# Optimization experiments

Hardware: AMD Instinct MI355X
Metric: run time of the kernel (lower is better)

Reference implementation:

```python
import jax, jax.numpy as jnp
import numpy as np
from jax import lax

B, T, F, H, NC = 64, 256, 64, 128, 2


def setup_inputs() -> dict:
    key = jax.random.key(0)
    ks = jax.random.split(key, 10)
    # timestamps: sorted ints with duplicates -> exercises per-timestamp mean aggregation
    t = jnp.sort(jax.random.randint(ks[0], (B, T), 0, T // 2), axis=1).astype(jnp.float32)
    m = jax.random.randint(ks[1], (B, T), 0, F).astype(jnp.float32)
    x = jax.random.normal(ks[2], (B, T), dtype=jnp.float32)
    delt = jax.random.uniform(ks[3], (B, T), dtype=jnp.float32)
    X = jnp.stack([t, m, x, delt], axis=1)  # [B, 4, T]
    lengths = jax.random.randint(ks[4], (B,), T // 2, T + 1).astype(jnp.int32)
    s = 1.0 / np.sqrt(H + 1)
    W_lin = jax.random.uniform(ks[5], (F, H + 1, 4 * H), minval=-s, maxval=s, dtype=jnp.float32)
    b_lin = jax.random.uniform(ks[6], (F, 4 * H), minval=-s, maxval=s, dtype=jnp.float32)
    W_dec = jax.random.uniform(ks[7], (F,), minval=-1.0, maxval=1.0, dtype=jnp.float32)
    b_dec = jax.random.uniform(ks[8], (F,), minval=-1.0, maxval=1.0, dtype=jnp.float32)
    so = 1.0 / np.sqrt(F * H + H)
    k9, k10 = jax.random.split(ks[9])
    W_out = jax.random.uniform(k9, (F * H + H, NC), minval=-so, maxval=so, dtype=jnp.float32)
    b_out = jax.random.uniform(k10, (NC,), minval=-so, maxval=so, dtype=jnp.float32)
    return {"X": X, "lengths": lengths, "W_lin": W_lin, "b_lin": b_lin,
            "W_dec": W_dec, "b_dec": b_dec, "W_out": W_out, "b_out": b_out}


def _forward(X, lengths, W_lin, b_lin, W_dec, b_dec, W_out, b_out):
    nF, Hp1, H4 = W_lin.shape
    hs = Hp1 - 1
    t = X[:, 0]
    m = X[:, 1].astype(jnp.int32)
    x = X[:, 2]
    delt = X[:, 3]
    idx = jnp.arange(t.shape[1])
    valid = idx[None, :] < lengths[:, None]                       # event is real
    t_next = jnp.concatenate([t[:, 1:], t[:, -1:] + 1.0], axis=1)
    # last event of a consecutive-equal-timestamp group (within valid length)
    boundary = (idx[None, :] == (lengths[:, None] - 1)) | (t_next != t)

    def per_sample(m_s, x_s, d_s, v_s, b_s):
        def step(carry, inp):
            h_t, c_t, acc, cnt = carry
            mj, xj, dj, vj, bj = inp
            # feature-specific decay of that feature's hidden row
            dm = W_dec[mj] * dj + b_dec[mj]
            decay = jnp.exp(-jnp.maximum(0.0, dm))
            h_dec = decay * h_t[mj]
            inp_vec = jnp.concatenate([xj[None], h_dec])          # [H+1]
            gates = inp_vec @ W_lin[mj] + b_lin[mj]               # [4H]
            gi, gf, go, gc = jnp.split(gates, 4)
            c_cand = jax.nn.sigmoid(gf) * c_t + jax.nn.sigmoid(gi) * jnp.tanh(gc)
            h_row = jax.nn.sigmoid(go) * jnp.tanh(c_cand)
            h_t = jnp.where(vj, h_t.at[mj].set(h_row), h_t)
            acc = acc + jnp.where(vj, c_cand, 0.0)
            cnt = cnt + jnp.where(vj, 1.0, 0.0)
            close = vj & bj                                       # end of timestamp group
            c_t = jnp.where(close, acc / jnp.maximum(cnt, 1.0), c_t)
            acc = jnp.where(close, jnp.zeros_like(acc), acc)
            cnt = jnp.where(close, 0.0, cnt)
            return (h_t, c_t, acc, cnt), None

        init = (jnp.zeros((nF, hs), jnp.float32), jnp.zeros((hs,), jnp.float32),
                jnp.zeros((hs,), jnp.float32), jnp.float32(0.0))
        (h_t, c_t, _, _), _ = lax.scan(step, init, (m_s, x_s, d_s, v_s, b_s))
        feats = jnp.concatenate([c_t, h_t.reshape(-1)])           # [H + F*H]
        return jax.nn.softmax(feats @ W_out + b_out)

    return jax.vmap(per_sample)(m, x, delt, valid, boundary)      # [B, n_class]


def reference(X, lengths, W_lin, b_lin, W_dec, b_dec, W_out, b_out):
    return _forward(X, lengths, W_lin, b_lin, W_dec, b_dec, W_out, b_out)
```

## Files before the change

### kernel.cpp

```cpp
#include <hip/hip_runtime.h>
#include <math.h>
#include <stdint.h>

#define BATCH 64
#define T 256
#define NF 64
#define H 128
#define H4 512
#define HP1 129
#define WF_STRIDE (HP1 * H4)
#define FEATS (NF * H + H)
#define NTH2 512

#define RING_SLOT 32768
#define PACK2_U4 (64 * 8 * 2 * 4 * 64)
#define PACK2_BYTES ((size_t)PACK2_U4 * 16u)
#define HDR2_BYTES  (64u * 512u * 16u)
#define WS_NEED ((size_t)HDR2_BYTES + PACK2_BYTES)

typedef float vf2 __attribute__((ext_vector_type(2)));

__device__ __forceinline__ float sigmoidf_(float x) {
    return 1.0f / (1.0f + __expf(-x));
}

__device__ __forceinline__ float tanhf_(float x) {
    float ax = fabsf(x);
    float e = __expf(2.0f * ax);
    float r = 1.0f - 2.0f / (e + 1.0f);
    return copysignf(r, x);
}

template<bool HI>
__device__ __forceinline__ vf2 dec2f(unsigned u) {
    return __builtin_amdgcn_cvt_pk_f32_fp8(u, HI);
}

__device__ __forceinline__ void dma16(const void* g, uint32_t lds_byte) {
    __builtin_amdgcn_global_load_lds(
        (const __attribute__((address_space(1))) void*)g,
        (__attribute__((address_space(3))) void*)(uintptr_t)lds_byte,
        16, 0, 0);
}

#define WAITV(N) do { asm volatile("s_waitcnt vmcnt(" #N ")" ::: "memory"); \
                      __builtin_amdgcn_sched_barrier(0); } while (0)
#define LGKM0()  do { asm volatile("s_waitcnt lgkmcnt(0)" ::: "memory"); \
                      __builtin_amdgcn_sched_barrier(0); } while (0)
#define BARRIER() do { asm volatile("s_waitcnt lgkmcnt(0)" ::: "memory"); \
                       __builtin_amdgcn_s_barrier(); \
                       asm volatile("" ::: "memory"); } while (0)

__global__ __launch_bounds__(256)
void repack2_kernel(const float* __restrict__ W_lin, uint4* __restrict__ pack2) {
    const int lin = blockIdx.x * 256 + threadIdx.x;
    const int l   = lin & 63;
    const int i   = (lin >> 6) & 3;
    const int Xv  = (lin >> 8) & 1;
    const int wv  = (lin >> 9) & 7;
    const int f   = lin >> 12;
    const int h   = wv * 16 + (l & 15);
    const int ks  = l >> 4;
    const int g   = Xv * 2 + (i >> 1);
    const int ksub = i & 1;
    const int col = g * 128 + h;
    const int k0  = ks * 32 + ksub * 16;
    const float* src = W_lin + (size_t)f * WF_STRIDE + (size_t)(1 + k0) * H4 + col;
    unsigned u[4];
    #pragma unroll
    for (int dw = 0; dw < 4; ++dw) {
        const float v0 = src[(4 * dw + 0) * H4] * 4096.0f;
        const float v1 = src[(4 * dw + 1) * H4] * 4096.0f;
        const float v2 = src[(4 * dw + 2) * H4] * 4096.0f;
        const float v3 = src[(4 * dw + 3) * H4] * 4096.0f;
        unsigned r = 0;
        r = __builtin_amdgcn_cvt_pk_fp8_f32(v0, v1, r, false);
        r = __builtin_amdgcn_cvt_pk_fp8_f32(v2, v3, r, true);
        u[dw] = r;
    }
    uint4 o; o.x = u[0]; o.y = u[1]; o.z = u[2]; o.w = u[3];
    pack2[lin] = o;
}

__global__ __launch_bounds__(256)
void hdr2_kernel(const float* __restrict__ W_lin, const float* __restrict__ b_lin,
                 uint4* __restrict__ hdr2) {
    const int lin = blockIdx.x * 256 + threadIdx.x;
    const int t2 = lin & 511, f = lin >> 9;
    const int wv = t2 >> 6, l = t2 & 63;
    const int h  = wv * 16 + (l & 15);
    union { uint4 u; _Float16 hf[8]; } o;
    #pragma unroll
    for (int g = 0; g < 4; ++g) {
        o.hf[g]     = (_Float16)W_lin[(size_t)f * WF_STRIDE + g * 128 + h];
        o.hf[4 + g] = (_Float16)b_lin[f * H4 + g * 128 + h];
    }
    hdr2[lin] = o.u;
}

__global__ __launch_bounds__(NTH2)
void lstm_scan_fp8_w1(const float* __restrict__ X,
                      const int* __restrict__ lengths,
                      const float* __restrict__ W_dec,
                      const float* __restrict__ b_dec,
                      const float* __restrict__ W_out,
                      const float* __restrict__ b_out,
                      const uint4* __restrict__ pack2,
                      const uint4* __restrict__ hdr2,
                      float* __restrict__ out)
{
    __shared__ __align__(16) char s_wb[3 * RING_SLOT];
    __shared__ __align__(16) char s_hd[2 * 8192];
    __shared__ float s_ht[NF * H];
    __shared__ float s_inp[H];
    __shared__ float s_X[4 * T];
    __shared__ float s_wdec[NF];
    __shared__ float s_bdec[NF];
    __shared__ float s_cfin[H];
    __shared__ float s_red[16];

    const int tid = threadIdx.x;
    const int b   = blockIdx.x;
    const int w   = tid >> 6;
    const int l   = tid & 63;
    const int h   = w * 16 + (l & 15);
    const int ks  = l >> 4;

    const float* Xb = X + b * 4 * T;
    const int len = lengths[b];

    for (int i = tid; i < NF * H; i += NTH2) s_ht[i] = 0.0f;
    for (int i = tid; i < 4 * T; i += NTH2) s_X[i] = Xb[i];
    if (tid < NF) { s_wdec[tid] = W_dec[tid]; s_bdec[tid] = b_dec[tid]; }
    if (tid < H) s_inp[tid] = 0.0f;
    __syncthreads();

    const uint32_t wb0 = (uint32_t)(uintptr_t)s_wb;
    const uint32_t hd0 = (uint32_t)(uintptr_t)s_hd;
    const uint32_t wbase  = __builtin_amdgcn_readfirstlane(wb0 + (uint32_t)w * 4096u);
    const uint32_t hdbase = __builtin_amdgcn_readfirstlane(hd0 + (uint32_t)w * 1024u);

    float c_t = 0.0f, accv = 0.0f, cntv = 0.0f;

    #define ISSUE_W4(mf, Xv, slot) do {                                          \
        const uint4* gp = pack2 + ((((size_t)(mf) * 8 + w) * 2 + (Xv)) * 4) * 64 + l; \
        const uint32_t dst = wbase + (uint32_t)(slot) * RING_SLOT;               \
        dma16(gp,       dst);                                                    \
        dma16(gp + 64,  dst + 1024u);                                            \
        dma16(gp + 128, dst + 2048u);                                            \
        dma16(gp + 192, dst + 3072u);                                            \
    } while (0)

    #define ISSUE_HDR(jj) do {                                                   \
        const int ss = ((jj) < T) ? (jj) : (T - 1);                              \
        const int mf = (int)s_X[T + ss];                                         \
        const uint4* gh = hdr2 + (size_t)mf * 512 + (w * 64 + l);                \
        dma16(gh, hdbase + (((jj) & 1) ? 8192u : 0u));                           \
    } while (0)

    #define DOTQ(Wq, G, KS) do {                                                 \
        const int pb = (KS) * 8;                                                 \
        vf2 d;                                                                   \
        d = dec2f<false>((Wq).x); acc[G] += d * iv[pb + 0];                      \
        d = dec2f<true >((Wq).x); acc[G] += d * iv[pb + 1];                      \
        d = dec2f<false>((Wq).y); acc[G] += d * iv[pb + 2];                      \
        d = dec2f<true >((Wq).y); acc[G] += d * iv[pb + 3];                      \
        d = dec2f<false>((Wq).z); acc[G] += d * iv[pb + 4];                      \
        d = dec2f<true >((Wq).z); acc[G] += d * iv[pb + 5];                      \
        d = dec2f<false>((Wq).w); acc[G] += d * iv[pb + 6];                      \
        d = dec2f<true >((Wq).w); acc[G] += d * iv[pb + 7];                      \
    } while (0)

    #define HALFX(Xv, slot) do {                                                 \
        uint4 q0, q1, q2, q3;                                                    \
        const uint32_t ra = wb0 + (uint32_t)(slot) * RING_SLOT                   \
                          + (uint32_t)w * 4096u + (uint32_t)l * 16u;             \
        asm volatile("ds_read_b128 %0, %4 offset:0\n\t"                          \
                     "ds_read_b128 %1, %4 offset:1024\n\t"                       \
                     "ds_read_b128 %2, %4 offset:2048\n\t"                       \
                     "ds_read_b128 %3, %4 offset:3072"                           \
                     : "=&v"(q0), "=&v"(q1), "=&v"(q2), "=&v"(q3)                \
                     : "v"(ra) : "memory");                                      \
        asm volatile("s_waitcnt lgkmcnt(0)" ::: "memory");                       \
        __builtin_amdgcn_sched_barrier(0);                                       \
        DOTQ(q0, (Xv) * 2 + 0, 0);                                               \
        DOTQ(q1, (Xv) * 2 + 0, 1);                                               \
        DOTQ(q2, (Xv) * 2 + 1, 0);                                               \
        DOTQ(q3, (Xv) * 2 + 1, 1);                                               \
    } while (0)

    {
        const int m0 = (int)s_X[T];
        ISSUE_W4(m0, 0, 0);
        ISSUE_HDR(0);
        ISSUE_W4(m0, 1, 1);
    }

    int r0 = 0;
    for (int j = 0; j < len; ++j) {
        const int   mj  = (int)s_X[T + j];
        const float xj  = s_X[2 * T + j];
        const int   jn  = (j + 1 < T) ? (j + 1) : (T - 1);
        const int   mjn = (int)s_X[T + jn];
        int r1 = r0 + 1; if (r1 >= 3) r1 -= 3;
        int r2 = r0 + 2; if (r2 >= 3) r2 -= 3;

        ISSUE_W4(mjn, 0, r2);
        ISSUE_HDR(j + 1);

        vf2 iv[16];
        {
            const float4* ip = (const float4*)(s_inp + ks * 32);
            #pragma unroll
            for (int q = 0; q < 8; ++q) {
                const float4 t = ip[q];
                iv[2 * q][0] = t.x;  iv[2 * q][1] = t.y;
                iv[2 * q + 1][0] = t.z; iv[2 * q + 1][1] = t.w;
            }
        }
        vf2 acc[4];
        #pragma unroll
        for (int g = 0; g < 4; ++g) { acc[g][0] = 0.0f; acc[g][1] = 0.0f; }

        WAITV(9);
        HALFX(0, r0);

        uint4 hb;
        {
            const uint32_t ha = hd0 + ((j & 1) ? 8192u : 0u)
                              + (uint32_t)w * 1024u + (uint32_t)l * 16u;
            asm volatile("ds_read_b128 %0, %1" : "=&v"(hb) : "v"(ha) : "memory");
        }
        LGKM0();
        ISSUE_W4(mjn, 1, r0);
        WAITV(9);
        HALFX(1, r1);

        union { uint4 u; _Float16 hf[8]; } hu; hu.u = hb;
        float gate[4];
        #pragma unroll
        for (int g = 0; g < 4; ++g) {
            float s = acc[g][0] + acc[g][1];
            s += __shfl_xor(s, 16, 64);
            s += __shfl_xor(s, 32, 64);
            gate[g] = fmaf(s, 1.0f / 4096.0f,
                           fmaf(xj, (float)hu.hf[g], (float)hu.hf[4 + g]));
        }
        const float c_cand = sigmoidf_(gate[1]) * c_t + sigmoidf_(gate[0]) * tanhf_(gate[3]);
        const float h_row  = sigmoidf_(gate[2]) * tanhf_(c_cand);
        accv += c_cand;
        cntv += 1.0f;
        const float tj = s_X[j];
        const float tn = (j < T - 1) ? s_X[j + 1] : (tj + 1.0f);
        const bool boundary = (j == len - 1) || (tn != tj);
        if (boundary) { c_t = accv / fmaxf(cntv, 1.0f); accv = 0.0f; cntv = 0.0f; }
        if ((l & 48) == 0) {
            s_ht[mj * H + h] = h_row;
            const float dn  = s_X[3 * T + jn];
            const float dmn = fmaf(s_wdec[mjn], dn, s_bdec[mjn]);
            const float den = __expf(-fmaxf(0.0f, dmn));
            const float hv  = (mjn == mj) ? h_row : s_ht[mjn * H + h];
            s_inp[h] = den * hv;
        }
        BARRIER();
        r0 = r2;
    }
    #undef HALFX
    #undef DOTQ
    #undef ISSUE_HDR
    #undef ISSUE_W4

    asm volatile("s_waitcnt vmcnt(0) lgkmcnt(0)" ::: "memory");
    __syncthreads();

    if ((l & 48) == 0) s_cfin[h] = c_t;
    __syncthreads();

    float z0 = 0.0f, z1 = 0.0f;
    for (int i = tid; i < FEATS; i += NTH2) {
        const float f = (i < H) ? s_cfin[i] : s_ht[i - H];
        const float2 wo = *(const float2*)(W_out + 2 * i);
        z0 = fmaf(f, wo.x, z0);
        z1 = fmaf(f, wo.y, z1);
    }
    #pragma unroll
    for (int off = 32; off > 0; off >>= 1) {
        z0 += __shfl_down(z0, off, 64);
        z1 += __shfl_down(z1, off, 64);
    }
    if (l == 0) { s_red[2 * w] = z0; s_red[2 * w + 1] = z1; }
    __syncthreads();
    if (tid == 0) {
        float a0 = b_out[0], a1 = b_out[1];
        #pragma unroll
        for (int q = 0; q < 8; ++q) { a0 += s_red[2 * q]; a1 += s_red[2 * q + 1]; }
        const float mx = fmaxf(a0, a1);
        const float e0 = __expf(a0 - mx), e1 = __expf(a1 - mx);
        const float inv = 1.0f / (e0 + e1);
        out[2 * b]     = e0 * inv;
        out[2 * b + 1] = e1 * inv;
    }
}

#define NTHREADS 512
__global__ __launch_bounds__(NTHREADS)
void lstm_scan_kernel(const float* __restrict__ X,
                      const int* __restrict__ lengths,
                      const float* __restrict__ W_lin,
                      const float* __restrict__ b_lin,
                      const float* __restrict__ W_dec,
                      const float* __restrict__ b_dec,
                      const float* __restrict__ W_out,
                      const float* __restrict__ b_out,
                      float* __restrict__ out)
{
    __shared__ float s_feats[FEATS];
    __shared__ float s_inp[H];
    __shared__ float s_part[4][H4];
    __shared__ float s_X[4 * T];
    __shared__ float s_wdec[NF];
    __shared__ float s_bdec[NF];
    __shared__ float s_red[16];

    float* s_ct = s_feats;
    float* s_ht = s_feats + H;

    const int tid = threadIdx.x;
    const int b   = blockIdx.x;
    const int g4  = tid & 127;
    const int kq  = tid >> 7;

    const float* Xb = X + b * 4 * T;
    const int len = lengths[b];

    for (int i = tid; i < NF * H; i += NTHREADS) s_ht[i] = 0.0f;
    for (int i = tid; i < 4 * T; i += NTHREADS) s_X[i] = Xb[i];
    if (tid < NF) { s_wdec[tid] = W_dec[tid]; s_bdec[tid] = b_dec[tid]; }
    __syncthreads();

    float c_t = 0.0f, acc = 0.0f, cnt = 0.0f;

    for (int j = 0; j < len; ++j) {
        const int   mj = (int)s_X[T + j];
        const float xj = s_X[2 * T + j];
        const float* Wf = W_lin + mj * WF_STRIDE;

        float bl0, bl1, bl2, bl3;
        if (tid < H) {
            const float dj    = s_X[3 * T + j];
            const float dm    = fmaf(s_wdec[mj], dj, s_bdec[mj]);
            const float decay = __expf(-fmaxf(0.0f, dm));
            s_inp[tid] = decay * s_ht[mj * H + tid];
            const int m4 = mj * H4;
            bl0 = b_lin[m4 + tid];
            bl1 = b_lin[m4 + H + tid];
            bl2 = b_lin[m4 + 2 * H + tid];
            bl3 = b_lin[m4 + 3 * H + tid];
        }
        __syncthreads();

        float4 a4 = make_float4(0.0f, 0.0f, 0.0f, 0.0f);
        {
            const float*  wr  = Wf + (1 + kq * 32) * H4 + 4 * g4;
            const float4* ivp = (const float4*)(s_inp + kq * 32);
            #pragma unroll
            for (int cc = 0; cc < 8; ++cc) {
                const float4 v = ivp[cc];
                const float* wrc = wr + (4 * cc) * H4;
                const float4 w0 = *(const float4*)(wrc);
                const float4 w1 = *(const float4*)(wrc + H4);
                const float4 w2 = *(const float4*)(wrc + 2 * H4);
                const float4 w3 = *(const float4*)(wrc + 3 * H4);
                a4.x = fmaf(v.x, w0.x, a4.x); a4.y = fmaf(v.x, w0.y, a4.y);
                a4.z = fmaf(v.x, w0.z, a4.z); a4.w = fmaf(v.x, w0.w, a4.w);
                a4.x = fmaf(v.y, w1.x, a4.x); a4.y = fmaf(v.y, w1.y, a4.y);
                a4.z = fmaf(v.y, w1.z, a4.z); a4.w = fmaf(v.y, w1.w, a4.w);
                a4.x = fmaf(v.z, w2.x, a4.x); a4.y = fmaf(v.z, w2.y, a4.y);
                a4.z = fmaf(v.z, w2.z, a4.z); a4.w = fmaf(v.z, w2.w, a4.w);
                a4.x = fmaf(v.w, w3.x, a4.x); a4.y = fmaf(v.w, w3.y, a4.y);
                a4.z = fmaf(v.w, w3.z, a4.z); a4.w = fmaf(v.w, w3.w, a4.w);
            }
        }
        if (kq == 0) {
            const float4 wv = *(const float4*)(Wf + 4 * g4);
            a4.x = fmaf(xj, wv.x, a4.x); a4.y = fmaf(xj, wv.y, a4.y);
            a4.z = fmaf(xj, wv.z, a4.z); a4.w = fmaf(xj, wv.w, a4.w);
        }
        *(float4*)(&s_part[kq][4 * g4]) = a4;
        __syncthreads();

        if (tid < H) {
            const int h = tid;
            const float gi = s_part[0][h]         + s_part[1][h]         + s_part[2][h]         + s_part[3][h]         + bl0;
            const float gf = s_part[0][H + h]     + s_part[1][H + h]     + s_part[2][H + h]     + s_part[3][H + h]     + bl1;
            const float go = s_part[0][2*H + h]   + s_part[1][2*H + h]   + s_part[2][2*H + h]   + s_part[3][2*H + h]   + bl2;
            const float gc = s_part[0][3*H + h]   + s_part[1][3*H + h]   + s_part[2][3*H + h]   + s_part[3][3*H + h]   + bl3;

            const float c_cand = sigmoidf_(gf) * c_t + sigmoidf_(gi) * tanhf_(gc);
            const float h_row  = sigmoidf_(go) * tanhf_(c_cand);
            s_ht[mj * H + h] = h_row;
            acc += c_cand;
            cnt += 1.0f;

            const float tj = s_X[j];
            const float tn = (j < T - 1) ? s_X[j + 1] : (tj + 1.0f);
            const bool boundary = (j == len - 1) || (tn != tj);
            if (boundary) { c_t = acc / fmaxf(cnt, 1.0f); acc = 0.0f; cnt = 0.0f; }
        }
        __syncthreads();
    }

    if (tid < H) s_ct[tid] = c_t;
    __syncthreads();

    float z0 = 0.0f, z1 = 0.0f;
    for (int i = tid; i < FEATS; i += NTHREADS) {
        const float f = s_feats[i];
        const float2 wv = *(const float2*)(W_out + 2 * i);
        z0 = fmaf(f, wv.x, z0);
        z1 = fmaf(f, wv.y, z1);
    }
    #pragma unroll
    for (int off = 32; off > 0; off >>= 1) {
        z0 += __shfl_down(z0, off, 64);
        z1 += __shfl_down(z1, off, 64);
    }
    const int wave = tid >> 6, lane = tid & 63;
    if (lane == 0) { s_red[2 * wave] = z0; s_red[2 * wave + 1] = z1; }
    __syncthreads();
    if (tid == 0) {
        float a0 = b_out[0], a1 = b_out[1];
        #pragma unroll
        for (int q = 0; q < 8; ++q) { a0 += s_red[2 * q]; a1 += s_red[2 * q + 1]; }
        const float mx = fmaxf(a0, a1);
        const float e0 = __expf(a0 - mx), e1 = __expf(a1 - mx);
        const float inv = 1.0f / (e0 + e1);
        out[2 * b]     = e0 * inv;
        out[2 * b + 1] = e1 * inv;
    }
}

extern "C" void kernel_launch(void* const* d_in, const int* in_sizes, int n_in,
                              void* d_out, int out_size, void* d_ws, size_t ws_size,
                              hipStream_t stream) {
    const float* X      = (const float*)d_in[0];
    const int*   lens   = (const int*)d_in[1];
    const float* W_lin  = (const float*)d_in[2];
    const float* b_lin  = (const float*)d_in[3];
    const float* W_dec  = (const float*)d_in[4];
    const float* b_dec  = (const float*)d_in[5];
    const float* W_out  = (const float*)d_in[6];
    const float* b_out  = (const float*)d_in[7];
    float* out = (float*)d_out;

    if (ws_size >= WS_NEED) {
        uint4* hdr2 = (uint4*)d_ws;
        uint4* pack2 = (uint4*)((char*)d_ws + HDR2_BYTES);
        hipLaunchKernelGGL(hdr2_kernel, dim3(128), dim3(256), 0, stream,
                           W_lin, b_lin, hdr2);
        hipLaunchKernelGGL(repack2_kernel, dim3(PACK2_U4 / 256), dim3(256), 0, stream,
                           W_lin, pack2);
        hipLaunchKernelGGL(lstm_scan_fp8_w1, dim3(BATCH), dim3(NTH2), 0, stream,
                           X, lens, W_dec, b_dec, W_out, b_out, pack2, hdr2, out);
    } else {
        hipLaunchKernelGGL(lstm_scan_kernel, dim3(BATCH), dim3(NTHREADS), 0, stream,
                           X, lens, W_lin, b_lin, W_dec, b_dec, W_out, b_out, out);
    }
}
```

Baseline: 507.6 us.

## Process two timesteps per iteration speculatively with two 512-thread groups

Replaces the single-step LSTM scan, which used an async LDS ring buffer for the weights, with a 1024-thread kernel. Two thread groups compute the matvecs for steps j and j+1 in parallel, and the second step is recomputed only when both steps hit the same feature row. Weights now load straight from global memory into registers instead of through the DMA prefetch ring. This halves the serial step count when features differ, at the cost of losing the prefetch overlap, adding extra barriers on collisions, and using larger blocks.

```diff
diff --git a/kernel.cpp b/kernel.cpp
--- a/kernel.cpp
+++ b/kernel.cpp
@@ -10,9 +10,8 @@
 #define HP1 129
 #define WF_STRIDE (HP1 * H4)
 #define FEATS (NF * H + H)
-#define NTH2 512
-
-#define RING_SLOT 32768
+#define NTH3 1024
+
 #define PACK2_U4 (64 * 8 * 2 * 4 * 64)
 #define PACK2_BYTES ((size_t)PACK2_U4 * 16u)
 #define HDR2_BYTES  (64u * 512u * 16u)
@@ -35,21 +34,6 @@
 __device__ __forceinline__ vf2 dec2f(unsigned u) {
     return __builtin_amdgcn_cvt_pk_f32_fp8(u, HI);
 }
-
-__device__ __forceinline__ void dma16(const void* g, uint32_t lds_byte) {
-    __builtin_amdgcn_global_load_lds(
-        (const __attribute__((address_space(1))) void*)g,
-        (__attribute__((address_space(3))) void*)(uintptr_t)lds_byte,
-        16, 0, 0);
-}
-
-#define WAITV(N) do { asm volatile("s_waitcnt vmcnt(" #N ")" ::: "memory"); \
-                      __builtin_amdgcn_sched_barrier(0); } while (0)
-#define LGKM0()  do { asm volatile("s_waitcnt lgkmcnt(0)" ::: "memory"); \
-                      __builtin_amdgcn_sched_barrier(0); } while (0)
-#define BARRIER() do { asm volatile("s_waitcnt lgkmcnt(0)" ::: "memory"); \
-                       __builtin_amdgcn_s_barrier(); \
-                       asm volatile("" ::: "memory"); } while (0)
 
 __global__ __launch_bounds__(256)
 void repack2_kernel(const float* __restrict__ W_lin, uint4* __restrict__ pack2) {
@@ -98,186 +82,197 @@
     hdr2[lin] = o.u;
 }
 
-__global__ __launch_bounds__(NTH2)
-void lstm_scan_fp8_w1(const float* __restrict__ X,
-                      const int* __restrict__ lengths,
-                      const float* __restrict__ W_dec,
-                      const float* __restrict__ b_dec,
-                      const float* __restrict__ W_out,
-                      const float* __restrict__ b_out,
-                      const uint4* __restrict__ pack2,
-                      const uint4* __restrict__ hdr2,
-                      float* __restrict__ out)
+__global__ __launch_bounds__(NTH3, 4)
+void lstm_scan_fp8_pair(const float* __restrict__ X,
+                        const int* __restrict__ lengths,
+                        const float* __restrict__ W_dec,
+                        const float* __restrict__ b_dec,
+                        const float* __restrict__ W_out,
+                        const float* __restrict__ b_out,
+                        const uint4* __restrict__ pack2,
+                        const uint4* __restrict__ hdr2,
+                        float* __restrict__ out)
 {
-    __shared__ __align__(16) char s_wb[3 * RING_SLOT];
-    __shared__ __align__(16) char s_hd[2 * 8192];
     __shared__ float s_ht[NF * H];
-    __shared__ float s_inp[H];
+    __shared__ float s_inpA[H];
+    __shared__ float s_inpB[H];
+    __shared__ float s_gates[2][H][4];
     __shared__ float s_X[4 * T];
     __shared__ float s_wdec[NF];
     __shared__ float s_bdec[NF];
     __shared__ float s_cfin[H];
-    __shared__ float s_red[16];
+    __shared__ float s_red[32];
 
     const int tid = threadIdx.x;
     const int b   = blockIdx.x;
-    const int w   = tid >> 6;
+    const int grp = tid >> 9;
+    const int w8  = (tid >> 6) & 7;
     const int l   = tid & 63;
-    const int h   = w * 16 + (l & 15);
+    const int h   = w8 * 16 + (l & 15);
     const int ks  = l >> 4;
 
     const float* Xb = X + b * 4 * T;
     const int len = lengths[b];
 
-    for (int i = tid; i < NF * H; i += NTH2) s_ht[i] = 0.0f;
-    for (int i = tid; i < 4 * T; i += NTH2) s_X[i] = Xb[i];
+    for (int i = tid; i < NF * H; i += NTH3) s_ht[i] = 0.0f;
+    for (int i = tid; i < 4 * T; i += NTH3) s_X[i] = Xb[i];
     if (tid < NF) { s_wdec[tid] = W_dec[tid]; s_bdec[tid] = b_dec[tid]; }
-    if (tid < H) s_inp[tid] = 0.0f;
-    __syncthreads();
-
-    const uint32_t wb0 = (uint32_t)(uintptr_t)s_wb;
-    const uint32_t hd0 = (uint32_t)(uintptr_t)s_hd;
-    const uint32_t wbase  = __builtin_amdgcn_readfirstlane(wb0 + (uint32_t)w * 4096u);
-    const uint32_t hdbase = __builtin_amdgcn_readfirstlane(hd0 + (uint32_t)w * 1024u);
+    if (tid < H) { s_inpA[tid] = 0.0f; s_inpB[tid] = 0.0f; }
+    __syncthreads();
 
     float c_t = 0.0f, accv = 0.0f, cntv = 0.0f;
 
-    #define ISSUE_W4(mf, Xv, slot) do {                                          \
-        const uint4* gp = pack2 + ((((size_t)(mf) * 8 + w) * 2 + (Xv)) * 4) * 64 + l; \
-        const uint32_t dst = wbase + (uint32_t)(slot) * RING_SLOT;               \
-        dma16(gp,       dst);                                                    \
-        dma16(gp + 64,  dst + 1024u);                                            \
-        dma16(gp + 128, dst + 2048u);                                            \
-        dma16(gp + 192, dst + 3072u);                                            \
+    #define DOTQ(Wq, G, KS) do {                                                \
+        const int pb = (KS) * 8;                                                \
+        vf2 d;                                                                  \
+        d = dec2f<false>((Wq).x); acc[G] += d * iv[pb + 0];                     \
+        d = dec2f<true >((Wq).x); acc[G] += d * iv[pb + 1];                     \
+        d = dec2f<false>((Wq).y); acc[G] += d * iv[pb + 2];                     \
+        d = dec2f<true >((Wq).y); acc[G] += d * iv[pb + 3];                     \
+        d = dec2f<false>((Wq).z); acc[G] += d * iv[pb + 4];                     \
+        d = dec2f<true >((Wq).z); acc[G] += d * iv[pb + 5];                     \
+        d = dec2f<false>((Wq).w); acc[G] += d * iv[pb + 6];                     \
+        d = dec2f<true >((Wq).w); acc[G] += d * iv[pb + 7];                     \
     } while (0)
 
-    #define ISSUE_HDR(jj) do {                                                   \
-        const int ss = ((jj) < T) ? (jj) : (T - 1);                              \
-        const int mf = (int)s_X[T + ss];                                         \
-        const uint4* gh = hdr2 + (size_t)mf * 512 + (w * 64 + l);                \
-        dma16(gh, hdbase + (((jj) & 1) ? 8192u : 0u));                           \
+    #define MATVEC(MF, INP, XV, GATE) do {                                      \
+        uint4 q[8];                                                             \
+        const uint4* wp_ = pack2 + (((size_t)(MF) * 8 + w8) * 2 * 4) * 64 + l;  \
+        _Pragma("unroll")                                                       \
+        for (int ii = 0; ii < 8; ++ii) q[ii] = wp_[ii * 64];                    \
+        union { uint4 u; _Float16 hf[8]; } hu_;                                 \
+        hu_.u = hdr2[(size_t)(MF) * 512 + (w8 * 64 + l)];                       \
+        vf2 iv[16];                                                             \
+        {                                                                       \
+            const float4* ip_ = (const float4*)((INP) + ks * 32);               \
+            _Pragma("unroll")                                                   \
+            for (int qd = 0; qd < 8; ++qd) {                                    \
+                const float4 t_ = ip_[qd];                                      \
+                iv[2 * qd][0] = t_.x;     iv[2 * qd][1] = t_.y;                 \
+                iv[2 * qd + 1][0] = t_.z; iv[2 * qd + 1][1] = t_.w;             \
+            }                                                                   \
+        }                                                                       \
+        vf2 acc[4];                                                             \
+        _Pragma("unroll")                                                       \
+        for (int g = 0; g < 4; ++g) { acc[g][0] = 0.0f; acc[g][1] = 0.0f; }     \
+        _Pragma("unroll")                                                       \
+        for (int Xi = 0; Xi < 2; ++Xi) {                                        \
+            DOTQ(q[Xi * 4 + 0], Xi * 2 + 0, 0);                                 \
+            DOTQ(q[Xi * 4 + 1], Xi * 2 + 0, 1);                                 \
+            DOTQ(q[Xi * 4 + 2], Xi * 2 + 1, 0);                                 \
+            DOTQ(q[Xi * 4 + 3], Xi * 2 + 1, 1);                                 \
+        }                                                                       \
+        _Pragma("unroll")                                                       \
+        for (int g = 0; g < 4; ++g) {                                           \
+            float s_ = acc[g][0] + acc[g][1];                                   \
+            s_ += __shfl_xor(s_, 16, 64);                                       \
+            s_ += __shfl_xor(s_, 32, 64);                                       \
+            GATE[g] = fmaf(s_, 1.0f / 4096.0f,                                  \
+                           fmaf((XV), (float)hu_.hf[g], (float)hu_.hf[4 + g])); \
+        }                                                                       \
     } while (0)
 
-    #define DOTQ(Wq, G, KS) do {                                                 \
-        const int pb = (KS) * 8;                                                 \
-        vf2 d;                                                                   \
-        d = dec2f<false>((Wq).x); acc[G] += d * iv[pb + 0];                      \
-        d = dec2f<true >((Wq).x); acc[G] += d * iv[pb + 1];                      \
-        d = dec2f<false>((Wq).y); acc[G] += d * iv[pb + 2];                      \
-        d = dec2f<true >((Wq).y); acc[G] += d * iv[pb + 3];                      \
-        d = dec2f<false>((Wq).z); acc[G] += d * iv[pb + 4];                      \
-        d = dec2f<true >((Wq).z); acc[G] += d * iv[pb + 5];                      \
-        d = dec2f<false>((Wq).w); acc[G] += d * iv[pb + 6];                      \
-        d = dec2f<true >((Wq).w); acc[G] += d * iv[pb + 7];                      \
-    } while (0)
-
-    #define HALFX(Xv, slot) do {                                                 \
-        uint4 q0, q1, q2, q3;                                                    \
-        const uint32_t ra = wb0 + (uint32_t)(slot) * RING_SLOT                   \
-                          + (uint32_t)w * 4096u + (uint32_t)l * 16u;             \
-        asm volatile("ds_read_b128 %0, %4 offset:0\n\t"                          \
-                     "ds_read_b128 %1, %4 offset:1024\n\t"                       \
-                     "ds_read_b128 %2, %4 offset:2048\n\t"                       \
-                     "ds_read_b128 %3, %4 offset:3072"                           \
-                     : "=&v"(q0), "=&v"(q1), "=&v"(q2), "=&v"(q3)                \
-                     : "v"(ra) : "memory");                                      \
-        asm volatile("s_waitcnt lgkmcnt(0)" ::: "memory");                       \
-        __builtin_amdgcn_sched_barrier(0);                                       \
-        DOTQ(q0, (Xv) * 2 + 0, 0);                                               \
-        DOTQ(q1, (Xv) * 2 + 0, 1);                                               \
-        DOTQ(q2, (Xv) * 2 + 1, 0);                                               \
-        DOTQ(q3, (Xv) * 2 + 1, 1);                                               \
-    } while (0)
-
-    {
-        const int m0 = (int)s_X[T];
-        ISSUE_W4(m0, 0, 0);
-        ISSUE_HDR(0);
-        ISSUE_W4(m0, 1, 1);
-    }
-
-    int r0 = 0;
-    for (int j = 0; j < len; ++j) {
-        const int   mj  = (int)s_X[T + j];
+    for (int j = 0; j < len; j += 2) {
+        const int  vj1 = (j + 1 < len);
+        const int  mj  = (int)s_X[T + j];
+        const int  j1c = (j + 1 < T) ? (j + 1) : (T - 1);
+        const int  mj1 = (int)s_X[T + j1c];
         const float xj  = s_X[2 * T + j];
-        const int   jn  = (j + 1 < T) ? (j + 1) : (T - 1);
-        const int   mjn = (int)s_X[T + jn];
-        int r1 = r0 + 1; if (r1 >= 3) r1 -= 3;
-        int r2 = r0 + 2; if (r2 >= 3) r2 -= 3;
-
-        ISSUE_W4(mjn, 0, r2);
-        ISSUE_HDR(j + 1);
-
-        vf2 iv[16];
+        const float xj1 = s_X[2 * T + j1c];
+
         {
-            const float4* ip = (const float4*)(s_inp + ks * 32);
-            #pragma unroll
-            for (int q = 0; q < 8; ++q) {
-                const float4 t = ip[q];
-                iv[2 * q][0] = t.x;  iv[2 * q][1] = t.y;
-                iv[2 * q + 1][0] = t.z; iv[2 * q + 1][1] = t.w;
+            const int   myM   = grp ? mj1 : mj;
+            const float myx   = grp ? xj1 : xj;
+            const float* myin = grp ? s_inpB : s_inpA;
+            float gate[4];
+            MATVEC(myM, myin, myx, gate);
+            if (ks == 0) {
+                float4 g4; g4.x = gate[0]; g4.y = gate[1]; g4.z = gate[2]; g4.w = gate[3];
+                *(float4*)&s_gates[grp][h][0] = g4;
             }
         }
-        vf2 acc[4];
-        #pragma unroll
-        for (int g = 0; g < 4; ++g) { acc[g][0] = 0.0f; acc[g][1] = 0.0f; }
-
-        WAITV(9);
-        HALFX(0, r0);
-
-        uint4 hb;
+        __syncthreads();
+
+        const float4 gA = *(const float4*)&s_gates[0][h][0];
+        float4 gB = *(const float4*)&s_gates[1][h][0];
+
+        const float c_candA = sigmoidf_(gA.y) * c_t + sigmoidf_(gA.x) * tanhf_(gA.w);
+        const float h_rowA  = sigmoidf_(gA.z) * tanhf_(c_candA);
+        accv += c_candA;
+        cntv += 1.0f;
         {
-            const uint32_t ha = hd0 + ((j & 1) ? 8192u : 0u)
-                              + (uint32_t)w * 1024u + (uint32_t)l * 16u;
-            asm volatile("ds_read_b128 %0, %1" : "=&v"(hb) : "v"(ha) : "memory");
-        }
-        LGKM0();
-        ISSUE_W4(mjn, 1, r0);
-        WAITV(9);
-        HALFX(1, r1);
-
-        union { uint4 u; _Float16 hf[8]; } hu; hu.u = hb;
-        float gate[4];
-        #pragma unroll
-        for (int g = 0; g < 4; ++g) {
-            float s = acc[g][0] + acc[g][1];
-            s += __shfl_xor(s, 16, 64);
-            s += __shfl_xor(s, 32, 64);
-            gate[g] = fmaf(s, 1.0f / 4096.0f,
-                           fmaf(xj, (float)hu.hf[g], (float)hu.hf[4 + g]));
-        }
-        const float c_cand = sigmoidf_(gate[1]) * c_t + sigmoidf_(gate[0]) * tanhf_(gate[3]);
-        const float h_row  = sigmoidf_(gate[2]) * tanhf_(c_cand);
-        accv += c_cand;
-        cntv += 1.0f;
-        const float tj = s_X[j];
-        const float tn = (j < T - 1) ? s_X[j + 1] : (tj + 1.0f);
-        const bool boundary = (j == len - 1) || (tn != tj);
-        if (boundary) { c_t = accv / fmaxf(cntv, 1.0f); accv = 0.0f; cntv = 0.0f; }
-        if ((l & 48) == 0) {
-            s_ht[mj * H + h] = h_row;
-            const float dn  = s_X[3 * T + jn];
-            const float dmn = fmaf(s_wdec[mjn], dn, s_bdec[mjn]);
-            const float den = __expf(-fmaxf(0.0f, dmn));
-            const float hv  = (mjn == mj) ? h_row : s_ht[mjn * H + h];
-            s_inp[h] = den * hv;
-        }
-        BARRIER();
-        r0 = r2;
-    }
-    #undef HALFX
+            const float tj  = s_X[j];
+            const float tn1 = (j < T - 1) ? s_X[j + 1] : (tj + 1.0f);
+            const bool bdry = (j == len - 1) || (tn1 != tj);
+            if (bdry) { c_t = accv / fmaxf(cntv, 1.0f); accv = 0.0f; cntv = 0.0f; }
+        }
+
+        const bool coll = vj1 && (mj1 == mj);
+        if (coll) {
+            const float d1  = s_X[3 * T + j1c];
+            const float dm1 = fmaf(s_wdec[mj1], d1, s_bdec[mj1]);
+            const float de1 = __expf(-fmaxf(0.0f, dm1));
+            if (grp == 1 && ks == 0) s_inpB[h] = de1 * h_rowA;
+            __syncthreads();
+            if (grp == 1) {
+                float gr[4];
+                MATVEC(mj1, s_inpB, xj1, gr);
+                if (ks == 0) {
+                    float4 g4; g4.x = gr[0]; g4.y = gr[1]; g4.z = gr[2]; g4.w = gr[3];
+                    *(float4*)&s_gates[1][h][0] = g4;
+                }
+            }
+            __syncthreads();
+            gB = *(const float4*)&s_gates[1][h][0];
+        }
+
+        float h_rowB = 0.0f;
+        if (vj1) {
+            const float c_candB = sigmoidf_(gB.y) * c_t + sigmoidf_(gB.x) * tanhf_(gB.w);
+            h_rowB = sigmoidf_(gB.z) * tanhf_(c_candB);
+            accv += c_candB;
+            cntv += 1.0f;
+            const float tj1 = s_X[j1c];
+            const float tn2 = (j + 1 < T - 1) ? s_X[j + 2] : (tj1 + 1.0f);
+            const bool bdry = (j + 1 == len - 1) || (tn2 != tj1);
+            if (bdry) { c_t = accv / fmaxf(cntv, 1.0f); accv = 0.0f; cntv = 0.0f; }
+        }
+
+        if (ks == 0) {
+            if (grp == 0 && !coll) s_ht[mj * H + h] = h_rowA;
+            if (grp == 1 && vj1)   s_ht[mj1 * H + h] = h_rowB;
+        }
+
+        const int j2 = (j + 2 < T) ? (j + 2) : (T - 1);
+        const int j3 = (j + 3 < T) ? (j + 3) : (T - 1);
+        const int m2 = (int)s_X[T + j2];
+        const int m3 = (int)s_X[T + j3];
+        if (ks == 0 && grp == 0) {
+            const float d2  = s_X[3 * T + j2];
+            const float dm2 = fmaf(s_wdec[m2], d2, s_bdec[m2]);
+            const float de2 = __expf(-fmaxf(0.0f, dm2));
+            const float hv2 = (vj1 && m2 == mj1) ? h_rowB
+                            : ((m2 == mj) ? h_rowA : s_ht[m2 * H + h]);
+            s_inpA[h] = de2 * hv2;
+        }
+        if (ks == 0 && grp == 1) {
+            const float d3  = s_X[3 * T + j3];
+            const float dm3 = fmaf(s_wdec[m3], d3, s_bdec[m3]);
+            const float de3 = __expf(-fmaxf(0.0f, dm3));
+            const float hv3 = (vj1 && m3 == mj1) ? h_rowB
+                            : ((m3 == mj) ? h_rowA : s_ht[m3 * H + h]);
+            s_inpB[h] = de3 * hv3;
+        }
+        __syncthreads();
+    }
+    #undef MATVEC
     #undef DOTQ
-    #undef ISSUE_HDR
-    #undef ISSUE_W4
-
-    asm volatile("s_waitcnt vmcnt(0) lgkmcnt(0)" ::: "memory");
-    __syncthreads();
-
-    if ((l & 48) == 0) s_cfin[h] = c_t;
+
+    if (grp == 0 && ks == 0) s_cfin[h] = c_t;
     __syncthreads();
 
     float z0 = 0.0f, z1 = 0.0f;
-    for (int i = tid; i < FEATS; i += NTH2) {
+    for (int i = tid; i < FEATS; i += NTH3) {
         const float f = (i < H) ? s_cfin[i] : s_ht[i - H];
         const float2 wo = *(const float2*)(W_out + 2 * i);
         z0 = fmaf(f, wo.x, z0);
@@ -288,12 +283,13 @@
         z0 += __shfl_down(z0, off, 64);
         z1 += __shfl_down(z1, off, 64);
     }
-    if (l == 0) { s_red[2 * w] = z0; s_red[2 * w + 1] = z1; }
+    const int wave = tid >> 6, lane2 = tid & 63;
+    if (lane2 == 0) { s_red[2 * wave] = z0; s_red[2 * wave + 1] = z1; }
     __syncthreads();
     if (tid == 0) {
         float a0 = b_out[0], a1 = b_out[1];
         #pragma unroll
-        for (int q = 0; q < 8; ++q) { a0 += s_red[2 * q]; a1 += s_red[2 * q + 1]; }
+        for (int q = 0; q < 16; ++q) { a0 += s_red[2 * q]; a1 += s_red[2 * q + 1]; }
         const float mx = fmaxf(a0, a1);
         const float e0 = __expf(a0 - mx), e1 = __expf(a1 - mx);
         const float inv = 1.0f / (e0 + e1);
@@ -460,7 +456,7 @@
                            W_lin, b_lin, hdr2);
         hipLaunchKernelGGL(repack2_kernel, dim3(PACK2_U4 / 256), dim3(256), 0, stream,
                            W_lin, pack2);
-        hipLaunchKernelGGL(lstm_scan_fp8_w1, dim3(BATCH), dim3(NTH2), 0, stream,
+        hipLaunchKernelGGL(lstm_scan_fp8_pair, dim3(BATCH), dim3(NTH3), 0, stream,
                            X, lens, W_dec, b_dec, W_out, b_out, pack2, hdr2, out);
     } else {
         hipLaunchKernelGGL(lstm_scan_kernel, dim3(BATCH), dim3(NTHREADS), 0, stream,
```

Result: slower. 542.8 us (+6.9%).
